# Kernel optimization log

Hardware: AMD Instinct MI355X
Metric: run time of the kernel (lower is better)

The kernel has to match this reference:

```python
import jax, jax.numpy as jnp
import numpy as np

N, E, F_IN, G = 50000, 800000, 128, 256
LAYERS = [(128, 4, 64), (256, 4, 64), (256, 1, 64)]  # (fan_in, heads, per-head dim)


def setup_inputs() -> dict:
    key = jax.random.key(0)
    ks = iter(jax.random.split(key, 64))
    nrm = lambda shp, s=1.0: jax.random.normal(next(ks), shp, jnp.float32) * s
    d = {}
    d["x"] = nrm((N, F_IN))
    d["edge_index"] = jax.random.randint(next(ks), (2, E), 0, N, dtype=jnp.int32)
    d["batch"] = jnp.sort(jax.random.randint(next(ks), (N,), 0, G, dtype=jnp.int32))
    for i, (fin, h, c) in enumerate(LAYERS):
        d[f"w{i}"] = nrm((fin, h * c), 1.0 / np.sqrt(fin))
        d[f"asrc{i}"] = nrm((h, c), 0.1)
        d[f"adst{i}"] = nrm((h, c), 0.1)
        d[f"b{i}"] = nrm((h * c,), 0.1)
        d[f"g{i}"] = 1.0 + nrm((h * c,), 0.1)
        d[f"be{i}"] = nrm((h * c,), 0.1)
        d[f"m{i}"] = nrm((h * c,), 0.1)
        d[f"v{i}"] = jnp.abs(nrm((h * c,), 0.1)) + 1.0
    d["fc1w"] = nrm((192, 64), 1.0 / np.sqrt(192)); d["fc1b"] = nrm((64,), 0.1)
    d["fc2w"] = nrm((64, 32), 1.0 / np.sqrt(64));   d["fc2b"] = nrm((32,), 0.1)
    d["fc3w"] = nrm((32, 1), 1.0 / np.sqrt(32));    d["fc3b"] = nrm((1,), 0.1)
    return d


def _gat_layer(x, w, a_s, a_d, b, src, dst, n, heads):
    c = w.shape[1] // heads
    h = (x @ w).reshape(n, heads, c)                      # [N,H,C]
    al_s = jnp.sum(h * a_s[None], axis=-1)                # [N,H]
    al_d = jnp.sum(h * a_d[None], axis=-1)                # [N,H]
    e = jax.nn.leaky_relu(al_s[src] + al_d[dst], 0.2)     # [E',H]
    emax = jax.ops.segment_max(e, dst, num_segments=n)
    emax = jnp.where(jnp.isfinite(emax), emax, 0.0)
    ee = jnp.exp(e - emax[dst])
    den = jax.ops.segment_sum(ee, dst, num_segments=n)
    alpha = ee / (den[dst] + 1e-16)                       # edge softmax per dst node
    out = jax.ops.segment_sum(h[src] * alpha[..., None], dst, num_segments=n)
    return out.reshape(n, heads * c) + b


def _bn(x, g, be, m, v):
    return (x - m) * jax.lax.rsqrt(v + 1e-5) * g + be


def reference(x, edge_index, batch,
              w0, asrc0, adst0, b0, g0, be0, m0, v0,
              w1, asrc1, adst1, b1, g1, be1, m1, v1,
              w2, asrc2, adst2, b2, g2, be2, m2, v2,
              fc1w, fc1b, fc2w, fc2b, fc3w, fc3b):
    n = x.shape[0]
    loop = jnp.arange(n, dtype=edge_index.dtype)          # add_self_loops (PyG default)
    src = jnp.concatenate([edge_index[0], loop])
    dst = jnp.concatenate([edge_index[1], loop])
    layers = [(w0, asrc0, adst0, b0, g0, be0, m0, v0, 4),
              (w1, asrc1, adst1, b1, g1, be1, m1, v1, 4),
              (w2, asrc2, adst2, b2, g2, be2, m2, v2, 1)]
    for (w, a_s, a_d, b, g, be, m, v, heads) in layers:
        x = _gat_layer(x, w, a_s, a_d, b, src, dst, n, heads)
        x = jax.nn.elu(_bn(x, g, be, m, v))
    # multi-pool readout over graphs
    xsum = jax.ops.segment_sum(x, batch, num_segments=G)
    cnt = jax.ops.segment_sum(jnp.ones((n, 1), x.dtype), batch, num_segments=G)
    xmean = xsum / jnp.maximum(cnt, 1.0)
    xmax = jax.ops.segment_max(x, batch, num_segments=G)
    xmax = jnp.where(jnp.isfinite(xmax), xmax, 0.0)
    h = jnp.concatenate([xmean, xmax, xsum], axis=1)      # [G, 192]
    h = jax.nn.relu(h @ fc1w + fc1b)
    h = jax.nn.relu(h @ fc2w + fc2b)
    return h @ fc3w + fc3b                                # [G, 1]
```

## Files before the change

kernel.cpp:

```cpp
#include <hip/hip_runtime.h>
#include <hip/hip_fp16.h>

typedef unsigned short ushort_t;
typedef unsigned int uint_t;
typedef __attribute__((ext_vector_type(8))) _Float16 half8;
typedef __attribute__((ext_vector_type(4))) float f32x4;

#define NN 50000
#define NE 800000
#define NGR 256

typedef __attribute__((address_space(3))) unsigned int as3_u32;
typedef const __attribute__((address_space(1))) unsigned int as1_u32c;
__device__ __forceinline__ void gld16(const ushort_t* g, void* lds_base) {
    __builtin_amdgcn_global_load_lds((as1_u32c*)g, (as3_u32*)lds_base, 16, 0, 0);
}

__global__ void k_scan1(const int* __restrict__ deg, int* __restrict__ rowp,
                        int* __restrict__ bsum, int M) {
    __shared__ int sm[256];
    int t = threadIdx.x, i = blockIdx.x * 256 + t;
    int v = (i < M) ? deg[i] + 1 : 0;
    sm[t] = v; __syncthreads();
    for (int off = 1; off < 256; off <<= 1) {
        int x = (t >= off) ? sm[t - off] : 0;
        __syncthreads();
        sm[t] += x;
        __syncthreads();
    }
    if (i < M) rowp[i] = sm[t] - v;
    if (t == 255) bsum[blockIdx.x] = sm[255];
}

__global__ void k_scan2(int* bsum, int NB) {
    __shared__ int sm[256];
    int t = threadIdx.x;
    int v = (t < NB) ? bsum[t] : 0;
    sm[t] = v; __syncthreads();
    for (int off = 1; off < 256; off <<= 1) {
        int x = (t >= off) ? sm[t - off] : 0;
        __syncthreads();
        sm[t] += x;
        __syncthreads();
    }
    if (t < NB) bsum[t] = sm[t] - v;
}

__global__ void k_scan3(int* rowp, const int* __restrict__ bsum, int* __restrict__ cur,
                        int M, int total) {
    int i = blockIdx.x * 256 + threadIdx.x;
    if (i < M) { rowp[i] += bsum[blockIdx.x]; cur[i] = 0; }
    if (i == 0) rowp[M] = total;
}

__global__ void k_prep(const float* __restrict__ x0, __half* __restrict__ xf,
                       const float* __restrict__ W0, const float* __restrict__ W1,
                       const float* __restrict__ W2, __half* __restrict__ th,
                       const int* __restrict__ edst, int* __restrict__ deg) {
    int i = blockIdx.x * 256 + threadIdx.x;
    if (i < 1600000) {
        float4 v = ((const float4*)x0)[i];
        __half2 a = __floats2half2_rn(v.x, v.y);
        __half2 b = __floats2half2_rn(v.z, v.w);
        *(__half2*)(xf + i * 4) = a;
        *(__half2*)(xf + i * 4 + 2) = b;
    } else if (i < 1600000 + 114688) {
        int w = i - 1600000;
        const float* W; int K, NC, idx, base;
        if (w < 32768)      { W = W0; K = 128; NC = 256; idx = w;         base = 0; }
        else if (w < 98304) { W = W1; K = 256; NC = 256; idx = w - 32768; base = 32768; }
        else                { W = W2; K = 256; NC = 64;  idx = w - 98304; base = 98304; }
        int k = idx / NC, n = idx % NC;
        th[base + n * K + k] = __float2half(W[idx]);
    } else if (i < 1600000 + 114688 + NE) {
        atomicAdd(&deg[edst[i - 1714688]], 1);
    }
}

template<int KD, int BN>
__device__ __forceinline__ void gemm_body(int bx, int by,
    const __half* __restrict__ Ax, const __half* __restrict__ Bth,
    __half* __restrict__ Hout, const float* __restrict__ a_s,
    const float* __restrict__ a_d, float* __restrict__ als,
    float* __restrict__ ald, int H, int M, int NC) {
    constexpr int BM = 128, BK = 32;
    __shared__ ushort_t sA[BM * BK];
    __shared__ ushort_t sB[BN * BK];
    const int tid = threadIdx.x;
    const int m0 = bx * BM;
    const int n0 = by * BN;
    const int wv = tid >> 6, ln = tid & 63;
    const int lrow = ln & 15, lq = ln >> 4;
    constexpr int RT = (BN == 128) ? 4 : 2;
    int wm, wn;
    if constexpr (BN == 128) { wm = (wv >> 1) * 64; wn = (wv & 1) * 64; }
    else                     { wm = wv * 32;        wn = 0; }
    const int roff = ln >> 2;
    const int coff = (ln & 3) * 8;

    f32x4 acc[RT][4] = {};

    for (int k0 = 0; k0 < KD; k0 += BK) {
        #pragma unroll
        for (int ch = 0; ch < 2; ++ch) {
            int rb = wv * 32 + ch * 16;
            size_t ga = (size_t)(m0 + rb + roff) * KD + k0 + coff;
            gld16((const ushort_t*)Ax + ga, &sA[rb * BK]);
        }
        if constexpr (BN == 128) {
            #pragma unroll
            for (int ch = 0; ch < 2; ++ch) {
                int rb = wv * 32 + ch * 16;
                size_t gb = (size_t)(n0 + rb + roff) * KD + k0 + coff;
                gld16((const ushort_t*)Bth + gb, &sB[rb * BK]);
            }
        } else {
            int rb = wv * 16;
            size_t gb = (size_t)(n0 + rb + roff) * KD + k0 + coff;
            gld16((const ushort_t*)Bth + gb, &sB[rb * BK]);
        }
        __syncthreads();
        half8 af[RT], bf[4];
        #pragma unroll
        for (int r = 0; r < RT; ++r)
            af[r] = *(const half8*)&sA[(wm + r * 16 + lrow) * BK + lq * 8];
        #pragma unroll
        for (int c = 0; c < 4; ++c)
            bf[c] = *(const half8*)&sB[(wn + c * 16 + lrow) * BK + lq * 8];
        #pragma unroll
        for (int r = 0; r < RT; ++r)
            #pragma unroll
            for (int c = 0; c < 4; ++c)
                acc[r][c] = __builtin_amdgcn_mfma_f32_16x16x32_f16(af[r], bf[c], acc[r][c], 0, 0, 0);
        __syncthreads();
    }
    #pragma unroll
    for (int r = 0; r < RT; ++r) {
        #pragma unroll
        for (int c = 0; c < 4; ++c) {
            int colg = n0 + wn + c * 16 + lrow;
            #pragma unroll
            for (int j = 0; j < 4; ++j) {
                int row = m0 + wm + r * 16 + lq * 4 + j;
                if (row < M) Hout[(size_t)row * NC + colg] = __float2half(acc[r][c][j]);
            }
        }
    }
    int hh = (n0 + wn) >> 6;
    float asv[4], adv[4];
    #pragma unroll
    for (int c = 0; c < 4; ++c) {
        int cg = (n0 + wn + c * 16 + lrow) & 63;
        asv[c] = a_s[hh * 64 + cg];
        adv[c] = a_d[hh * 64 + cg];
    }
    #pragma unroll
    for (int r = 0; r < RT; ++r) {
        #pragma unroll
        for (int j = 0; j < 4; ++j) {
            float ts = 0.f, td = 0.f;
            #pragma unroll
            for (int c = 0; c < 4; ++c) {
                float v = acc[r][c][j];
                ts += v * asv[c];
                td += v * adv[c];
            }
            #pragma unroll
            for (int m = 1; m < 16; m <<= 1) {
                ts += __shfl_xor(ts, m);
                td += __shfl_xor(td, m);
            }
            int row = m0 + wm + r * 16 + lq * 4 + j;
            if (lrow == 0 && row < M) {
                als[row * H + hh] = ts;
                ald[row * H + hh] = td;
            }
        }
    }
}

template<int KD, int BN>
__global__ __launch_bounds__(256)
void k_mgemm(const __half* __restrict__ Ax, const __half* __restrict__ Bth,
             __half* __restrict__ Hout,
             const float* __restrict__ a_s, const float* __restrict__ a_d,
             float* __restrict__ als, float* __restrict__ ald,
             int H, int M, int NC) {
    gemm_body<KD, BN>(blockIdx.x, blockIdx.y, Ax, Bth, Hout, a_s, a_d, als, ald, H, M, NC);
}

__global__ __launch_bounds__(256)
void k_gf(const __half* __restrict__ Ax, const __half* __restrict__ Bth,
          __half* __restrict__ Hout,
          const float* __restrict__ a_s, const float* __restrict__ a_d,
          float* __restrict__ als, float* __restrict__ ald, int M,
          const int* __restrict__ esrc, const int* __restrict__ edst,
          const int* __restrict__ rowp, int* __restrict__ cur,
          int* __restrict__ colv) {
    if (blockIdx.x < 782) {
        gemm_body<128, 128>(blockIdx.x >> 1, blockIdx.x & 1, Ax, Bth, Hout,
                            a_s, a_d, als, ald, 4, M, 256);
    } else {
        int i = (blockIdx.x - 782) * 256 + threadIdx.x;
        if (i < NE) {
            int d = edst[i];
            int pos = rowp[d] + atomicAdd(&cur[d], 1);
            colv[pos] = esrc[i];
        } else if (i < NE + NN) {
            int nn = i - NE;
            int pos = rowp[nn] + atomicAdd(&cur[nn], 1);
            colv[pos] = nn;
        }
    }
}

template<int H>
__global__ __launch_bounds__(256)
void k_att(const float* __restrict__ als, const float* __restrict__ ald,
           const int* __restrict__ rowp, const int* __restrict__ colv,
           __half* __restrict__ alpha, float* __restrict__ invb, int M) {
    int node = blockIdx.x * 16 + (threadIdx.x >> 4);
    if (node >= M) return;
    int l = threadIdx.x & 15;
    int rs = rowp[node], re = rowp[node + 1];
    if constexpr (H == 4) {
        float4 ad = *(const float4*)(ald + node * 4);
        float d0 = 0.f, d1 = 0.f, d2 = 0.f, d3 = 0.f;
        for (int i = rs + l; i < re; i += 16) {
            int s = colv[i];
            float4 av = *(const float4*)(als + s * 4);
            float e0 = av.x + ad.x; e0 = e0 > 0.f ? e0 : 0.2f * e0; e0 = __expf(e0);
            float e1 = av.y + ad.y; e1 = e1 > 0.f ? e1 : 0.2f * e1; e1 = __expf(e1);
            float e2 = av.z + ad.z; e2 = e2 > 0.f ? e2 : 0.2f * e2; e2 = __expf(e2);
            float e3 = av.w + ad.w; e3 = e3 > 0.f ? e3 : 0.2f * e3; e3 = __expf(e3);
            d0 += e0; d1 += e1; d2 += e2; d3 += e3;
            __half2 p0 = __floats2half2_rn(e0, e1);
            __half2 p1 = __floats2half2_rn(e2, e3);
            uint2 pk;
            pk.x = *(uint_t*)&p0; pk.y = *(uint_t*)&p1;
            *(uint2*)(alpha + (size_t)i * 4) = pk;
        }
        #pragma unroll
        for (int off = 1; off < 16; off <<= 1) {
            d0 += __shfl_xor(d0, off); d1 += __shfl_xor(d1, off);
            d2 += __shfl_xor(d2, off); d3 += __shfl_xor(d3, off);
        }
        if (l == 0)
            *(float4*)(invb + node * 4) = make_float4(1.f / (d0 + 1e-16f), 1.f / (d1 + 1e-16f),
                                                      1.f / (d2 + 1e-16f), 1.f / (d3 + 1e-16f));
    } else {
        float ad = ald[node];
        float d = 0.f;
        for (int i = rs + l; i < re; i += 16) {
            int s = colv[i];
            float e = als[s] + ad; e = e > 0.f ? e : 0.2f * e; e = __expf(e);
            d += e;
            alpha[i] = __float2half(e);
        }
        #pragma unroll
        for (int off = 1; off < 16; off <<= 1) d += __shfl_xor(d, off);
        if (l == 0) invb[node] = 1.f / (d + 1e-16f);
    }
}

template<int H, bool SPLIT>
__global__ __launch_bounds__(256)
void k_agg(const __half* __restrict__ h, const __half* __restrict__ alpha,
           const float* __restrict__ invb, const int* __restrict__ rowp,
           const int* __restrict__ colv,
           const float* __restrict__ bias, const float* __restrict__ gam,
           const float* __restrict__ bet, const float* __restrict__ mu,
           const float* __restrict__ var,
           __half* __restrict__ xo, float* __restrict__ xf, int M) {
    constexpr int HC = H * 64;
    constexpr int EG = 512 / HC;
    constexpr int L  = 64 / EG;
    constexpr int UN = (H == 4) ? 4 : 2;
    int node = blockIdx.x * 4 + (threadIdx.x >> 6);
    if (node >= M) return;
    int lane = threadIdx.x & 63;
    int rs = rowp[node], re = rowp[node + 1];
    int l = lane & (L - 1), eg = lane / L;
    int hB = (l * 8) >> 6;
    const ushort_t* ab = (const ushort_t*)alpha;
    float acc[8] = {};
    for (int i = rs; i < re; i += EG * UN) {
        #pragma unroll
        for (int k = 0; k < UN; ++k) {
            int idx = i + eg + k * EG;
            bool vld = idx < re;
            int idx2 = vld ? idx : rs;
            int s = colv[idx2];
            ushort_t abits;
            if constexpr (H == 4) abits = ab[(size_t)idx2 * 4 + hB];
            else                  abits = ab[idx2];
            float a = __half2float(__ushort_as_half(vld ? abits : (ushort_t)0));
            uint4 hv = *(const uint4*)(h + (size_t)s * HC + l * 8);
            const __half* hp = (const __half*)&hv;
            #pragma unroll
            for (int j = 0; j < 8; ++j)
                acc[j] = fmaf(a, __half2float(hp[j]), acc[j]);
        }
    }
    #pragma unroll
    for (int off = L; off < 64; off <<= 1) {
        #pragma unroll
        for (int j = 0; j < 8; ++j) acc[j] += __shfl_xor(acc[j], off);
    }
    if (eg == 0) {
        float inv = (H == 4) ? invb[node * 4 + hB] : invb[node];
        float fo[8];
        #pragma unroll
        for (int j = 0; j < 8; ++j) {
            int d = l * 8 + j;
            float o = acc[j] * inv + bias[d];
            float bn = (o - mu[d]) * rsqrtf(var[d] + 1e-5f) * gam[d] + bet[d];
            fo[j] = bn > 0.f ? bn : (__expf(bn) - 1.f);
        }
        if constexpr (SPLIT) {
            __half2 p0 = __floats2half2_rn(fo[0], fo[1]);
            __half2 p1 = __floats2half2_rn(fo[2], fo[3]);
            __half2 p2 = __floats2half2_rn(fo[4], fo[5]);
            __half2 p3 = __floats2half2_rn(fo[6], fo[7]);
            uint4 pk;
            pk.x = *(uint_t*)&p0; pk.y = *(uint_t*)&p1;
            pk.z = *(uint_t*)&p2; pk.w = *(uint_t*)&p3;
            *(uint4*)&xo[(size_t)node * HC + l * 8] = pk;
        } else {
            *(float4*)&xf[(size_t)node * HC + l * 8] = make_float4(fo[0], fo[1], fo[2], fo[3]);
            *(float4*)&xf[(size_t)node * HC + l * 8 + 4] = make_float4(fo[4], fo[5], fo[6], fo[7]);
        }
    }
}

__global__ __launch_bounds__(512)
void k_poolfc(const float* __restrict__ x, const int* __restrict__ batch,
              const float* __restrict__ fc1w, const float* __restrict__ fc1b,
              const float* __restrict__ fc2w, const float* __restrict__ fc2b,
              const float* __restrict__ fc3w, const float* __restrict__ fc3b,
              float* __restrict__ out, int M) {
    __shared__ float ssum[8][64];
    __shared__ float smax[8][64];
    __shared__ float hb[192];
    __shared__ float h1[64];
    __shared__ float h2[32];
    int g = blockIdx.x, t = threadIdx.x;
    int d = t & 63, sub = t >> 6;
    int lo = 0, hi = M;
    while (lo < hi) { int mid = (lo + hi) >> 1; if (batch[mid] < g) lo = mid + 1; else hi = mid; }
    int s = lo;
    lo = 0; hi = M;
    while (lo < hi) { int mid = (lo + hi) >> 1; if (batch[mid] < g + 1) lo = mid + 1; else hi = mid; }
    int e = lo;
    float sum = 0.f, mx = -3.0e38f;
    for (int n = s + sub; n < e; n += 8) {
        float v = x[(size_t)n * 64 + d];
        sum += v; mx = fmaxf(mx, v);
    }
    ssum[sub][d] = sum; smax[sub][d] = mx;
    __syncthreads();
    if (t < 64) {
        float sm = 0.f, m2 = -3.0e38f;
        #pragma unroll
        for (int k = 0; k < 8; ++k) { sm += ssum[k][t]; m2 = fmaxf(m2, smax[k][t]); }
        int cnt = e - s;
        hb[t] = sm / (float)(cnt > 1 ? cnt : 1);
        hb[64 + t] = (cnt == 0) ? 0.f : m2;
        hb[128 + t] = sm;
    }
    __syncthreads();
    if (t < 64) {
        float s1 = fc1b[t];
        for (int k = 0; k < 192; ++k) s1 += hb[k] * fc1w[k * 64 + t];
        h1[t] = fmaxf(s1, 0.f);
    }
    __syncthreads();
    if (t < 32) {
        float s2 = fc2b[t];
        for (int k = 0; k < 64; ++k) s2 += h1[k] * fc2w[k * 32 + t];
        h2[t] = fmaxf(s2, 0.f);
    }
    __syncthreads();
    if (t == 0) {
        float s3 = fc3b[0];
        for (int k = 0; k < 32; ++k) s3 += h2[k] * fc3w[k];
        out[g] = s3;
    }
}

extern "C" void kernel_launch(void* const* d_in, const int* in_sizes, int n_in,
                              void* d_out, int out_size, void* d_ws, size_t ws_size,
                              hipStream_t stream) {
    const float* x0     = (const float*)d_in[0];
    const int* ei       = (const int*)d_in[1];
    const int* batch    = (const int*)d_in[2];
    const float* W[3]   = {(const float*)d_in[3],  (const float*)d_in[11], (const float*)d_in[19]};
    const float* AS[3]  = {(const float*)d_in[4],  (const float*)d_in[12], (const float*)d_in[20]};
    const float* AD[3]  = {(const float*)d_in[5],  (const float*)d_in[13], (const float*)d_in[21]};
    const float* BI[3]  = {(const float*)d_in[6],  (const float*)d_in[14], (const float*)d_in[22]};
    const float* GA[3]  = {(const float*)d_in[7],  (const float*)d_in[15], (const float*)d_in[23]};
    const float* BE[3]  = {(const float*)d_in[8],  (const float*)d_in[16], (const float*)d_in[24]};
    const float* MU[3]  = {(const float*)d_in[9],  (const float*)d_in[17], (const float*)d_in[25]};
    const float* VA[3]  = {(const float*)d_in[10], (const float*)d_in[18], (const float*)d_in[26]};
    const float* fc1w = (const float*)d_in[27];
    const float* fc1b = (const float*)d_in[28];
    const float* fc2w = (const float*)d_in[29];
    const float* fc2b = (const float*)d_in[30];
    const float* fc3w = (const float*)d_in[31];
    const float* fc3b = (const float*)d_in[32];

    char* ws = (char*)d_ws;
    int*   rowp   = (int*)  (ws);
    int*   colv   = (int*)  (ws + 200704);
    int*   bsum   = (int*)  (ws + 3600704);
    float* als    = (float*)(ws + 3602432);
    float* ald    = (float*)(ws + 4402432);
    __half* wTh   = (__half*)(ws + 5202432);
    __half* h_buf = (__half*)(ws + 5661184);
    __half* xf16  = (__half*)(ws + 31261184);
    float* xpool  = (float*)(ws + 56885760);
    __half* alpha = (__half*)(ws + 69685760);
    float* invb   = (float*)(ws + 83285760);
    int*   cur    = (int*)  (ws + 84085760);

    const int* esrc = ei;
    const int* edst = ei + NE;
    const int NB_SCAN = (NN + 255) / 256;

    hipMemsetAsync(cur, 0, NN * sizeof(int), stream);
    k_prep<<<(1600000 + 114688 + NE + 255) / 256, 256, 0, stream>>>(x0, xf16, W[0], W[1], W[2],
                                                                    wTh, edst, cur);
    k_scan1<<<NB_SCAN, 256, 0, stream>>>(cur, rowp, bsum, NN);
    k_scan2<<<1, 256, 0, stream>>>(bsum, NB_SCAN);
    k_scan3<<<NB_SCAN, 256, 0, stream>>>(rowp, bsum, cur, NN, NE + NN);

    const int GB = (NN + 127) / 128;
    const int FILLB = (NE + NN + 255) / 256;
    int nwb = (NN + 3) / 4;
    int nab = (NN + 15) / 16;

    k_gf<<<782 + FILLB, 256, 0, stream>>>(xf16, wTh, h_buf, AS[0], AD[0], als, ald, NN,
                                          esrc, edst, rowp, cur, colv);
    k_att<4><<<nab, 256, 0, stream>>>(als, ald, rowp, colv, alpha, invb, NN);
    k_agg<4, true><<<nwb, 256, 0, stream>>>(h_buf, alpha, invb, rowp, colv,
                                            BI[0], GA[0], BE[0], MU[0], VA[0],
                                            xf16, nullptr, NN);
    k_mgemm<256, 128><<<dim3(GB, 2), 256, 0, stream>>>(xf16, wTh + 32768, h_buf,
                                                       AS[1], AD[1], als, ald, 4, NN, 256);
    k_att<4><<<nab, 256, 0, stream>>>(als, ald, rowp, colv, alpha, invb, NN);
    k_agg<4, true><<<nwb, 256, 0, stream>>>(h_buf, alpha, invb, rowp, colv,
                                            BI[1], GA[1], BE[1], MU[1], VA[1],
                                            xf16, nullptr, NN);
    k_mgemm<256, 64><<<dim3(GB, 1), 256, 0, stream>>>(xf16, wTh + 98304, h_buf,
                                                      AS[2], AD[2], als, ald, 1, NN, 64);
    k_att<1><<<nab, 256, 0, stream>>>(als, ald, rowp, colv, alpha, invb, NN);
    k_agg<1, false><<<nwb, 256, 0, stream>>>(h_buf, alpha, invb, rowp, colv,
                                             BI[2], GA[2], BE[2], MU[2], VA[2],
                                             nullptr, xpool, NN);

    k_poolfc<<<NGR, 512, 0, stream>>>(xpool, batch, fc1w, fc1b, fc2w, fc2b, fc3w, fc3b,
                                      (float*)d_out, NN);
    (void)in_sizes; (void)n_in; (void)out_size; (void)ws_size;
}
```

Baseline: 458.9 us.

## Partition CSR fill by destination range and prefill self-loops in scan

Self-loop entries are now written during the final scan pass, and the cursor is initialised to the absolute row start plus one, so the fill needs no rowp lookup. Each fill block loads four edges with vectorised int4 loads and inserts only the edges whose destination lies in one of eight node ranges. This keeps the atomic and colv writes of concurrent blocks within a narrower address window. In exchange every edge is read eight times, and the number of fill blocks grows accordingly.

```diff
diff --git a/kernel.cpp b/kernel.cpp
--- a/kernel.cpp
+++ b/kernel.cpp
@@ -47,9 +47,14 @@
 }
 
 __global__ void k_scan3(int* rowp, const int* __restrict__ bsum, int* __restrict__ cur,
-                        int M, int total) {
+                        int* __restrict__ colv, int M, int total) {
     int i = blockIdx.x * 256 + threadIdx.x;
-    if (i < M) { rowp[i] += bsum[blockIdx.x]; cur[i] = 0; }
+    if (i < M) {
+        int rp = rowp[i] + bsum[blockIdx.x];
+        rowp[i] = rp;
+        colv[rp] = i;
+        cur[i] = rp + 1;
+    }
     if (i == 0) rowp[M] = total;
 }
 
@@ -195,21 +200,29 @@
           const float* __restrict__ a_s, const float* __restrict__ a_d,
           float* __restrict__ als, float* __restrict__ ald, int M,
           const int* __restrict__ esrc, const int* __restrict__ edst,
-          const int* __restrict__ rowp, int* __restrict__ cur,
-          int* __restrict__ colv) {
+          int* __restrict__ cur, int* __restrict__ colv) {
     if (blockIdx.x < 782) {
         gemm_body<128, 128>(blockIdx.x >> 1, blockIdx.x & 1, Ax, Bth, Hout,
                             a_s, a_d, als, ald, 4, M, 256);
     } else {
-        int i = (blockIdx.x - 782) * 256 + threadIdx.x;
-        if (i < NE) {
-            int d = edst[i];
-            int pos = rowp[d] + atomicAdd(&cur[d], 1);
-            colv[pos] = esrc[i];
-        } else if (i < NE + NN) {
-            int nn = i - NE;
-            int pos = rowp[nn] + atomicAdd(&cur[nn], 1);
-            colv[pos] = nn;
+        int fid = blockIdx.x - 782;
+        int r = blockIdx.x & 7;
+        int c = fid >> 3;
+        int base = c * 1024 + (int)threadIdx.x * 4;
+        if (base < NE) {
+            int4 dv = *(const int4*)(edst + base);
+            int4 sv = *(const int4*)(esrc + base);
+            const int lo = r * 6250;
+            const int* dp = (const int*)&dv;
+            const int* sp = (const int*)&sv;
+            #pragma unroll
+            for (int j = 0; j < 4; ++j) {
+                int d = dp[j];
+                if ((unsigned)(d - lo) < 6250u) {
+                    int pos = atomicAdd(&cur[d], 1);
+                    colv[pos] = sp[j];
+                }
+            }
         }
     }
 }
@@ -432,15 +445,15 @@
                                                                     wTh, edst, cur);
     k_scan1<<<NB_SCAN, 256, 0, stream>>>(cur, rowp, bsum, NN);
     k_scan2<<<1, 256, 0, stream>>>(bsum, NB_SCAN);
-    k_scan3<<<NB_SCAN, 256, 0, stream>>>(rowp, bsum, cur, NN, NE + NN);
+    k_scan3<<<NB_SCAN, 256, 0, stream>>>(rowp, bsum, cur, colv, NN, NE + NN);
 
     const int GB = (NN + 127) / 128;
-    const int FILLB = (NE + NN + 255) / 256;
+    const int FILLB = ((NE + 1023) / 1024) * 8;
     int nwb = (NN + 3) / 4;
     int nab = (NN + 15) / 16;
 
     k_gf<<<782 + FILLB, 256, 0, stream>>>(xf16, wTh, h_buf, AS[0], AD[0], als, ald, NN,
-                                          esrc, edst, rowp, cur, colv);
+                                          esrc, edst, cur, colv);
     k_att<4><<<nab, 256, 0, stream>>>(als, ald, rowp, colv, alpha, invb, NN);
     k_agg<4, true><<<nwb, 256, 0, stream>>>(h_buf, alpha, invb, rowp, colv,
                                             BI[0], GA[0], BE[0], MU[0], VA[0],
```

New measurement: 459.4 us. No clear change (+0.1%).
